# Kernel optimization log

Hardware: AMD Instinct MI355X
Metric: run time of the kernel (lower is better)

## Reference

```python
import jax, jax.numpy as jnp
import numpy as np

HS = 2048   # hidden_size
NH = 16     # num_attention_heads
HD = HS // NH  # head_dim = 128
FD = 256    # feature_dim
EPS = 1e-5  # layer_norm_epsilon


def setup_inputs() -> dict:
    key = jax.random.key(0)
    ks = jax.random.split(key, 12)
    s = 0.02
    return {
        "hidden_states": jax.random.normal(ks[0], (2, 4096, HS), jnp.float32),
        "attention_mask": jnp.zeros((2, 4096), jnp.float32),
        "Wq": jax.random.normal(ks[1], (HS, HS), jnp.float32) * s,
        "bq": jnp.zeros((HS,), jnp.float32),
        "Wk": jax.random.normal(ks[2], (HS, HS), jnp.float32) * s,
        "bk": jnp.zeros((HS,), jnp.float32),
        "Wv": jax.random.normal(ks[3], (HS, HS), jnp.float32) * s,
        "bv": jnp.zeros((HS,), jnp.float32),
        "Wo": jax.random.normal(ks[4], (HS, HS), jnp.float32) * s,
        "bo": jnp.zeros((HS,), jnp.float32),
        "Wf1": jax.random.normal(ks[5], (HD, FD), jnp.float32) * s,
        "bf1": jnp.zeros((FD,), jnp.float32),
        "Wf2": jax.random.normal(ks[6], (FD, FD), jnp.float32) * s,
        "bf2": jnp.zeros((FD,), jnp.float32),
        "ln_g": jnp.ones((FD,), jnp.float32),
        "ln_b": jnp.zeros((FD,), jnp.float32),
    }


def reference(hidden_states, attention_mask, Wq, bq, Wk, bk, Wv, bv, Wo, bo,
              Wf1, bf1, Wf2, bf2, ln_g, ln_b):
    B, L, H = hidden_states.shape

    # QKV projections -> [B, NH, L, HD]
    q = (hidden_states @ Wq + bq).reshape(B, L, NH, HD).transpose(0, 2, 1, 3)
    k = (hidden_states @ Wk + bk).reshape(B, L, NH, HD).transpose(0, 2, 1, 3)
    v = (hidden_states @ Wv + bv).reshape(B, L, NH, HD).transpose(0, 2, 1, 3)

    # seq_len (4096) > linear_threshold (1024) -> linear attention branch
    def feature_map(x):  # Linear -> ReLU -> Linear -> LayerNorm
        h = jax.nn.relu(x @ Wf1 + bf1)
        h = h @ Wf2 + bf2
        mu = jnp.mean(h, axis=-1, keepdims=True)
        var = jnp.var(h, axis=-1, keepdims=True)  # biased, like torch LayerNorm
        return (h - mu) * jax.lax.rsqrt(var + EPS) * ln_g + ln_b

    q_feat = feature_map(q)  # [B, NH, L, FD]
    k_feat = feature_map(k)
    # attention_mask [B, L] -> k_feat * (1 + mask)
    k_feat = k_feat * (1.0 + attention_mask[:, None, :, None])

    kv = jnp.einsum('bhlf,bhld->bhfd', k_feat, v)          # [B, NH, FD, HD]
    attn = jnp.einsum('bhlf,bhfd->bhld', q_feat, kv)       # [B, NH, L, HD]
    k_sum = jnp.sum(k_feat, axis=2)                         # [B, NH, FD]
    denom = jnp.einsum('bhlf,bhf->bhl', q_feat, k_sum)[..., None]
    attn = attn / (denom + 1e-8)

    attn = attn.transpose(0, 2, 1, 3).reshape(B, L, H)
    return attn @ Wo + bo
```

## Files before the change

### kernel.cpp

```cpp
#include <hip/hip_runtime.h>

typedef unsigned short u16;
typedef unsigned int u32;
typedef __attribute__((ext_vector_type(8))) short bf16x8;
typedef __attribute__((ext_vector_type(4))) float f32x4;

#define B_ 2
#define L_ 4096
#define HS_ 2048
#define NH_ 16
#define HD_ 128
#define FD_ 256

__device__ __forceinline__ float bf2f(u16 u) { return __uint_as_float(((u32)u) << 16); }
__device__ __forceinline__ u16 f2bf(float f) {
    u32 x = __float_as_uint(f);
    return (u16)((x + 0x7fffu + ((x >> 16) & 1u)) >> 16);
}

__device__ __forceinline__ void llds16(const u16* g, u16* l) {
    __builtin_amdgcn_global_load_lds((const __attribute__((address_space(1))) void*)g,
                                     (__attribute__((address_space(3))) void*)l, 16, 0, 0);
}

__device__ __forceinline__ void gemm_mainloop(const u16* __restrict__ Ab, int lda,
                                              const u16* __restrict__ Bb, int ldb,
                                              int K, u16* As, u16* Bs, f32x4 (&acc)[4][4]) {
    const int tid  = threadIdx.x;
    const int lane = tid & 63;
    const int wave = tid >> 6;
    const int wm = wave >> 1, wn = wave & 1;

    f32x4 zero = {0.f, 0.f, 0.f, 0.f};
#pragma unroll
    for (int i = 0; i < 4; i++)
#pragma unroll
        for (int j = 0; j < 4; j++) acc[i][j] = zero;

    const int srow = lane >> 2;
    const int scol = (lane & 3) * 8;
    const u16* pa = Ab + (size_t)(wave * 32 + srow) * lda + scol;
    const u16* pb = Bb + (size_t)(wave * 32 + srow) * ldb + scol;
    u16* la = As + wave * 1024;
    u16* lb = Bs + wave * 1024;

    const int arow = (wm * 64 + (lane & 15)) * 32 + (lane >> 4) * 8;
    const int brow = (wn * 64 + (lane & 15)) * 32 + (lane >> 4) * 8;

    for (int k0 = 0; k0 < K; k0 += 32) {
        llds16(pa, la);
        llds16(pa + 16 * lda, la + 512);
        llds16(pb, lb);
        llds16(pb + 16 * ldb, lb + 512);
        pa += 32; pb += 32;
        __syncthreads();
        bf16x8 af[4], bg[4];
#pragma unroll
        for (int mt = 0; mt < 4; mt++) af[mt] = *(const bf16x8*)(As + arow + mt * 512);
#pragma unroll
        for (int nt = 0; nt < 4; nt++) bg[nt] = *(const bf16x8*)(Bs + brow + nt * 512);
#pragma unroll
        for (int mt = 0; mt < 4; mt++)
#pragma unroll
            for (int nt = 0; nt < 4; nt++)
                acc[mt][nt] = __builtin_amdgcn_mfma_f32_16x16x32_bf16(af[mt], bg[nt], acc[mt][nt], 0, 0, 0);
        __syncthreads();
    }
}

__global__ __launch_bounds__(256) void k_cvt(const float* __restrict__ src, u16* __restrict__ dst) {
    size_t i = ((size_t)blockIdx.x * 256 + threadIdx.x) * 8;
    float4 a = *(const float4*)(src + i);
    float4 b = *(const float4*)(src + i + 4);
    union { u16 h[8]; uint4 v; } o;
    o.h[0] = f2bf(a.x); o.h[1] = f2bf(a.y); o.h[2] = f2bf(a.z); o.h[3] = f2bf(a.w);
    o.h[4] = f2bf(b.x); o.h[5] = f2bf(b.y); o.h[6] = f2bf(b.z); o.h[7] = f2bf(b.w);
    *(uint4*)(dst + i) = o.v;
}

__global__ __launch_bounds__(256) void k_transpose(const float* Wq, const float* Wk, const float* Wv,
                                                   const float* Wo, const float* Wf1, const float* Wf2,
                                                   u16* Wqkv_t, u16* Wo_t, u16* Wf1_t, u16* Wf2_t) {
    const float* src; u16* dst; int R, C;
    switch (blockIdx.z) {
        case 0: src = Wq;  dst = Wqkv_t;                R = 2048; C = 2048; break;
        case 1: src = Wk;  dst = Wqkv_t + 2048 * 2048;  R = 2048; C = 2048; break;
        case 2: src = Wv;  dst = Wqkv_t + 2 * 2048 * 2048; R = 2048; C = 2048; break;
        case 3: src = Wo;  dst = Wo_t;                  R = 2048; C = 2048; break;
        case 4: src = Wf1; dst = Wf1_t;                 R = 128;  C = 256;  break;
        default: src = Wf2; dst = Wf2_t;                R = 256;  C = 256;  break;
    }
    int c0 = blockIdx.x * 32, r0 = blockIdx.y * 32;
    if (c0 >= C || r0 >= R) return;
    __shared__ u16 tile[32][33];
    int tx = threadIdx.x, ty = threadIdx.y;
    for (int i = ty; i < 32; i += 8) tile[i][tx] = f2bf(src[(size_t)(r0 + i) * C + c0 + tx]);
    __syncthreads();
    for (int i = ty; i < 32; i += 8) dst[(size_t)(c0 + i) * R + r0 + tx] = tile[tx][i];
}

#define QKV_BAR() { __builtin_amdgcn_sched_barrier(0); __builtin_amdgcn_s_barrier(); \
                    __builtin_amdgcn_sched_barrier(0); }
#define QKV_LGKM0() { asm volatile("s_waitcnt lgkmcnt(0)" ::: "memory"); \
                      __builtin_amdgcn_sched_barrier(0); }

__device__ __forceinline__ void mainloop256(const u16* __restrict__ Abase,
                                            const u16* __restrict__ Bbase,
                                            u16* LDS, f32x4 (&acc)[8][4]) {
    const int tid = threadIdx.x, lane = tid & 63, wave = tid >> 6;
    const int wm = wave >> 2, wn = wave & 3;

    int r0g, c0g, r1g, c1g;
    { int p = tid * 16; int s = p >> 10, q = p & 1023; q ^= ((q >> 9) & 1) << 5;
      r0g = (s >> 1) * 16 + (q >> 6); c0g = (s & 1) * 32 + ((q & 63) >> 1); }
    { int p = 8192 + tid * 16; int s = p >> 10, q = p & 1023; q ^= ((q >> 9) & 1) << 5;
      r1g = (s >> 1) * 16 + (q >> 6); c1g = (s & 1) * 32 + ((q & 63) >> 1); }
    const int voff0 = r0g * HS_ + c0g;
    const int voff1 = r1g * HS_ + c1g;

    int qby = (lane & 15) * 64 + (lane >> 4) * 16;
    qby ^= ((qby >> 9) & 1) << 5;
    const int qh = qby >> 1;

#define STG(G, soff, dstu) { \
    llds16((G) + (soff) + voff0, LDS + (dstu) + wave * 512); \
    llds16((G) + (soff) + voff1, LDS + (dstu) + 4096 + wave * 512); }

    const size_t a0 = 0, a1 = (size_t)128 * HS_;
    const size_t b0 = 0, b1 = (size_t)128 * HS_;

    STG(Bbase, b0, 32768); STG(Bbase, b1, 40960);
    STG(Abase, a0, 0);     STG(Abase, a1, 8192);
    STG(Bbase, b0 + 64, 49152); STG(Bbase, b1 + 64, 57344);
    STG(Abase, a0 + 64, 16384);
    asm volatile("s_waitcnt vmcnt(6)" ::: "memory");
    QKV_BAR();

    f32x4 zero = {0.f, 0.f, 0.f, 0.f};
#pragma unroll
    for (int i = 0; i < 8; i++)
#pragma unroll
        for (int j = 0; j < 4; j++) acc[i][j] = zero;

    const int NT = HS_ / 64;
    bf16x8 afr[4][2], bfr[4][2];
    for (int t = 0; t < NT; t++) {
        const int bsel = t & 1;
        const u16* Ah = LDS + bsel * 16384 + wm * 8192;
        const u16* Bh = LDS + 32768 + bsel * 16384 + (wn >> 1) * 8192;
        const int bg0 = (wn & 1) * 4;
        const size_t kc1 = (size_t)(t + 1) * 64, kc2 = (size_t)(t + 2) * 64;

#pragma unroll
        for (int mf = 0; mf < 4; mf++)
#pragma unroll
            for (int ks = 0; ks < 2; ks++)
                afr[mf][ks] = *(const bf16x8*)(Ah + (mf * 2 + ks) * 512 + qh);
#pragma unroll
        for (int nf = 0; nf < 4; nf++)
#pragma unroll
            for (int ks = 0; ks < 2; ks++)
                bfr[nf][ks] = *(const bf16x8*)(Bh + ((bg0 + nf) * 2 + ks) * 512 + qh);
        if (t + 1 < NT) STG(Abase, a1 + kc1, (bsel ^ 1) * 16384 + 8192);
        QKV_BAR();
        QKV_LGKM0();
        __builtin_amdgcn_s_setprio(1);
#pragma unroll
        for (int mf = 0; mf < 4; mf++)
#pragma unroll
            for (int nf = 0; nf < 2; nf++)
#pragma unroll
                for (int ks = 0; ks < 2; ks++)
                    acc[mf][nf] = __builtin_amdgcn_mfma_f32_16x16x32_bf16(afr[mf][ks], bfr[nf][ks], acc[mf][nf], 0, 0, 0);
        __builtin_amdgcn_s_setprio(0);
        QKV_BAR();
        if (t + 2 < NT) STG(Bbase, b0 + kc2, 32768 + bsel * 16384);
        QKV_BAR();
        __builtin_amdgcn_s_setprio(1);
#pragma unroll
        for (int mf = 0; mf < 4; mf++)
#pragma unroll
            for (int nf = 2; nf < 4; nf++)
#pragma unroll
                for (int ks = 0; ks < 2; ks++)
                    acc[mf][nf] = __builtin_amdgcn_mfma_f32_16x16x32_bf16(afr[mf][ks], bfr[nf][ks], acc[mf][nf], 0, 0, 0);
        __builtin_amdgcn_s_setprio(0);
        QKV_BAR();
#pragma unroll
        for (int mf = 0; mf < 4; mf++)
#pragma unroll
            for (int ks = 0; ks < 2; ks++)
                afr[mf][ks] = *(const bf16x8*)(Ah + ((mf + 4) * 2 + ks) * 512 + qh);
        if (t + 2 < NT) STG(Bbase, b1 + kc2, 32768 + bsel * 16384 + 8192);
        QKV_BAR();
        QKV_LGKM0();
        __builtin_amdgcn_s_setprio(1);
#pragma unroll
        for (int mf = 0; mf < 4; mf++)
#pragma unroll
            for (int nf = 0; nf < 2; nf++)
#pragma unroll
                for (int ks = 0; ks < 2; ks++)
                    acc[mf + 4][nf] = __builtin_amdgcn_mfma_f32_16x16x32_bf16(afr[mf][ks], bfr[nf][ks], acc[mf + 4][nf], 0, 0, 0);
        __builtin_amdgcn_s_setprio(0);
        QKV_BAR();
        if (t + 2 < NT) STG(Abase, a0 + kc2, bsel * 16384);
        QKV_BAR();
        __builtin_amdgcn_s_setprio(1);
#pragma unroll
        for (int mf = 0; mf < 4; mf++)
#pragma unroll
            for (int nf = 2; nf < 4; nf++)
#pragma unroll
                for (int ks = 0; ks < 2; ks++)
                    acc[mf + 4][nf] = __builtin_amdgcn_mfma_f32_16x16x32_bf16(afr[mf][ks], bfr[nf][ks], acc[mf + 4][nf], 0, 0, 0);
        __builtin_amdgcn_s_setprio(0);
        if (t + 2 < NT) { asm volatile("s_waitcnt vmcnt(6)" ::: "memory"); }
        else if (t + 1 < NT) { asm volatile("s_waitcnt vmcnt(0)" ::: "memory"); }
        QKV_BAR();
    }
#undef STG
}

__global__ __launch_bounds__(512, 2) void k_gemm_qkv(
        const u16* __restrict__ X, const u16* __restrict__ Wt,
        const float* __restrict__ bq, const float* __restrict__ bk, const float* __restrict__ bv,
        u16* __restrict__ qout, u16* __restrict__ kout, u16* __restrict__ vT) {
    __shared__ u16 LDS[65536];
    const int tid = threadIdx.x, lane = tid & 63, wave = tid >> 6;
    const int wm = wave >> 2, wn = wave & 3;

    const int xcd = blockIdx.x & 7, idx = blockIdx.x >> 3;
    const int nblk = idx >> 2;
    const int mblk = xcd * 4 + (idx & 3);
    const int mb = mblk * 256, nb = nblk * 256;

    f32x4 acc[8][4];
    mainloop256(X + (size_t)mb * HS_, Wt + (size_t)nb * HS_, LDS, acc);

    const int which = nblk >> 3;
    const int colbase = (nblk & 7) * 256;
    const int bi = mb >> 12, lb = mb & 4095;
    const float* bias = (which == 0) ? bq : (which == 1 ? bk : bv);
    const int rb = (lane >> 4) << 2, cl = lane & 15;

    if (which < 2) {
        u16* dst = (which == 0) ? qout : kout;
        const int bh0 = bi * NH_ + (colbase >> 7);
        for (int half = 0; half < 2; half++) {
            if (wm == half) {
#pragma unroll
                for (int nf = 0; nf < 4; nf++) {
                    float bvv = bias[colbase + wn * 64 + nf * 16 + cl];
#pragma unroll
                    for (int mf = 0; mf < 8; mf++)
#pragma unroll
                        for (int r = 0; r < 4; r++)
                            LDS[(mf * 16 + rb + r) * 264 + wn * 64 + nf * 16 + cl] =
                                f2bf(acc[mf][nf][r] + bvv);
                }
            }
            __syncthreads();
#pragma unroll
            for (int it = 0; it < 8; it++) {
                int row = (tid >> 5) + it * 16;
                int c8 = (tid & 31) * 8;
                uint2 lo = *(const uint2*)(LDS + row * 264 + c8);
                uint2 hi = *(const uint2*)(LDS + row * 264 + c8 + 4);
                uint4 val = make_uint4(lo.x, lo.y, hi.x, hi.y);
                u16* pp = dst + ((size_t)(bh0 + (c8 >> 7)) * L_ + lb + half * 128 + row) * HD_ + (c8 & 127);
                *(uint4*)pp = val;
            }
            __syncthreads();
        }
    } else {
        for (int half = 0; half < 2; half++) {
            if (wm == half) {
#pragma unroll
                for (int nf = 0; nf < 4; nf++) {
                    float bvv = bias[colbase + wn * 64 + nf * 16 + cl];
#pragma unroll
                    for (int mf = 0; mf < 8; mf++)
#pragma unroll
                        for (int r = 0; r < 4; r++)
                            LDS[(wn * 64 + nf * 16 + cl) * 136 + mf * 16 + rb + r] =
                                f2bf(acc[mf][nf][r] + bvv);
                }
            }
            __syncthreads();
#pragma unroll
            for (int it = 0; it < 8; it++) {
                int n = (tid >> 4) + it * 32;
                int c8 = (tid & 15) * 8;
                uint2 lo = *(const uint2*)(LDS + n * 136 + c8);
                uint2 hi = *(const uint2*)(LDS + n * 136 + c8 + 4);
                uint4 val = make_uint4(lo.x, lo.y, hi.x, hi.y);
                int cg = colbase + n;
                u16* pp = vT + ((size_t)(bi * NH_ + (cg >> 7)) * HD_ + (cg & 127)) * L_ + lb + half * 128 + c8;
                *(uint4*)pp = val;
            }
            __syncthreads();
        }
    }
}

__global__ __launch_bounds__(512, 2) void k_gemm_out(const u16* __restrict__ A, const u16* __restrict__ Wt,
                                                     const float* __restrict__ bo, float* __restrict__ out) {
    __shared__ u16 LDS[65536];
    const int lane = threadIdx.x & 63, wave = threadIdx.x >> 6;
    const int wm = wave >> 2, wn = wave & 3;

    const int xcd = blockIdx.x & 7, idx = blockIdx.x >> 3;
    const int nblk = idx >> 2;
    const int mblk = xcd * 4 + (idx & 3);
    const int mb = mblk * 256, nb = nblk * 256;

    f32x4 acc[8][4];
    mainloop256(A + (size_t)mb * HS_, Wt + (size_t)nb * HS_, LDS, acc);

    const int rb = (lane >> 4) << 2, cl = lane & 15;
#pragma unroll
    for (int nf = 0; nf < 4; nf++) {
        int n = nb + wn * 64 + nf * 16 + cl;
        float bvv = bo[n];
#pragma unroll
        for (int mf = 0; mf < 8; mf++) {
            int m = mb + wm * 128 + mf * 16 + rb;
#pragma unroll
            for (int r = 0; r < 4; r++)
                out[(size_t)(m + r) * HS_ + n] = acc[mf][nf][r] + bvv;
        }
    }
}

template <int MASKED, int TRANS>
__global__ __launch_bounds__(256) void k_feat(const u16* __restrict__ X,
                                              const u16* __restrict__ W1t, const float* __restrict__ b1,
                                              const u16* __restrict__ W2t, const float* __restrict__ b2,
                                              const float* __restrict__ g, const float* __restrict__ be,
                                              const float* __restrict__ mask,
                                              u16* __restrict__ feat, float* __restrict__ ksp) {
    __shared__ u16 As[64 * 32];
    __shared__ u16 Bs[256 * 32];
    __shared__ u16 H[64 * 264];
    __shared__ float MU[64], RS[64], FAC[64];
    const int tid = threadIdx.x, lane = tid & 63, wave = tid >> 6;
    const int mb = blockIdx.x * 64;

    const int srow = lane >> 2, scol = (lane & 3) * 8;
    const int arow_rd = (lane & 15);
    const int kgrp = (lane >> 4) * 8;

    f32x4 acc[4][4];
    f32x4 zero = {0.f, 0.f, 0.f, 0.f};
#pragma unroll
    for (int i = 0; i < 4; i++)
#pragma unroll
        for (int j = 0; j < 4; j++) acc[i][j] = zero;

    for (int k0 = 0; k0 < 128; k0 += 32) {
        llds16(X + (size_t)(mb + wave * 16 + srow) * 128 + k0 + scol, As + wave * 512);
#pragma unroll
        for (int i = 0; i < 4; i++)
            llds16(W1t + (size_t)((wave * 4 + i) * 16 + srow) * 128 + k0 + scol,
                   Bs + (wave * 4 + i) * 512);
        __syncthreads();
        bf16x8 af[4], bg[4];
#pragma unroll
        for (int mt = 0; mt < 4; mt++) af[mt] = *(const bf16x8*)(As + (mt * 16 + arow_rd) * 32 + kgrp);
#pragma unroll
        for (int nt = 0; nt < 4; nt++) bg[nt] = *(const bf16x8*)(Bs + (wave * 64 + nt * 16 + arow_rd) * 32 + kgrp);
#pragma unroll
        for (int mt = 0; mt < 4; mt++)
#pragma unroll
            for (int nt = 0; nt < 4; nt++)
                acc[mt][nt] = __builtin_amdgcn_mfma_f32_16x16x32_bf16(af[mt], bg[nt], acc[mt][nt], 0, 0, 0);
        __syncthreads();
    }
    {
        const int rbase = (lane >> 4) << 2;
#pragma unroll
        for (int nt = 0; nt < 4; nt++) {
            int n = wave * 64 + nt * 16 + (lane & 15);
            float bvv = b1[n];
#pragma unroll
            for (int mt = 0; mt < 4; mt++)
#pragma unroll
                for (int r = 0; r < 4; r++) {
                    float v = fmaxf(acc[mt][nt][r] + bvv, 0.f);
                    H[(mt * 16 + rbase + r) * 264 + n] = f2bf(v);
                }
            acc[0][nt] = zero; acc[1][nt] = zero; acc[2][nt] = zero; acc[3][nt] = zero;
        }
    }
    __syncthreads();

    for (int k0 = 0; k0 < 256; k0 += 32) {
#pragma unroll
        for (int i = 0; i < 4; i++)
            llds16(W2t + (size_t)((wave * 4 + i) * 16 + srow) * 256 + k0 + scol,
                   Bs + (wave * 4 + i) * 512);
        __syncthreads();
        bf16x8 af[4], bg[4];
#pragma unroll
        for (int mt = 0; mt < 4; mt++) af[mt] = *(const bf16x8*)(H + (mt * 16 + arow_rd) * 264 + k0 + kgrp);
#pragma unroll
        for (int nt = 0; nt < 4; nt++) bg[nt] = *(const bf16x8*)(Bs + (wave * 64 + nt * 16 + arow_rd) * 32 + kgrp);
#pragma unroll
        for (int mt = 0; mt < 4; mt++)
#pragma unroll
            for (int nt = 0; nt < 4; nt++)
                acc[mt][nt] = __builtin_amdgcn_mfma_f32_16x16x32_bf16(af[mt], bg[nt], acc[mt][nt], 0, 0, 0);
        __syncthreads();
    }
    {
        const int rbase = (lane >> 4) << 2;
#pragma unroll
        for (int nt = 0; nt < 4; nt++) {
            int n = wave * 64 + nt * 16 + (lane & 15);
            float bvv = b2[n];
#pragma unroll
            for (int mt = 0; mt < 4; mt++)
#pragma unroll
                for (int r = 0; r < 4; r++)
                    H[(mt * 16 + rbase + r) * 264 + n] = f2bf(acc[mt][nt][r] + bvv);
        }
    }
    __syncthreads();

    {
        for (int r = 0; r < 16; r++) {
            int row = wave * 16 + r;
            int j = lane * 4;
            uint2 u = *(const uint2*)(H + row * 264 + j);
            float x0 = bf2f((u16)(u.x & 0xffff)), x1 = bf2f((u16)(u.x >> 16));
            float x2 = bf2f((u16)(u.y & 0xffff)), x3 = bf2f((u16)(u.y >> 16));
            float s = x0 + x1 + x2 + x3;
            float ss = x0 * x0 + x1 * x1 + x2 * x2 + x3 * x3;
#pragma unroll
            for (int o = 32; o >= 1; o >>= 1) { s += __shfl_xor(s, o); ss += __shfl_xor(ss, o); }
            if (lane == 0) {
                float mu = s * (1.f / FD_);
                float var = ss * (1.f / FD_) - mu * mu;
                MU[row] = mu;
                RS[row] = rsqrtf(var + 1e-5f);
                float fac = 1.f;
                if (MASKED) {
                    int grow = mb + row;
                    int b = grow >> 16;
                    int l = grow & 4095;
                    fac = 1.f + mask[b * L_ + l];
                }
                FAC[row] = fac;
            }
        }
    }
    __syncthreads();

    if (!TRANS) {
        int j = lane * 4;
        float4 gg = *(const float4*)(g + j);
        float4 bb = *(const float4*)(be + j);
        for (int r = 0; r < 16; r++) {
            int row = wave * 16 + r;
            float mu = MU[row], rstd = RS[row], fac = FAC[row];
            uint2 u = *(const uint2*)(H + row * 264 + j);
            float x0 = bf2f((u16)(u.x & 0xffff)), x1 = bf2f((u16)(u.x >> 16));
            float x2 = bf2f((u16)(u.y & 0xffff)), x3 = bf2f((u16)(u.y >> 16));
            uint2 o2;
            o2.x = (u32)f2bf(((x0 - mu) * rstd * gg.x + bb.x) * fac) |
                   ((u32)f2bf(((x1 - mu) * rstd * gg.y + bb.y) * fac) << 16);
            o2.y = (u32)f2bf(((x2 - mu) * rstd * gg.z + bb.z) * fac) |
                   ((u32)f2bf(((x3 - mu) * rstd * gg.w + bb.w) * fac) << 16);
            *(uint2*)(feat + (size_t)(mb + row) * FD_ + j) = o2;
        }
    } else {
        int f = tid;
        int bh = mb >> 12, lb = mb & 4095;
        float gf = g[f], bf = be[f];
        u16* orow = feat + ((size_t)bh * FD_ + f) * L_ + lb;
        float fsum = 0.f;
        for (int lg = 0; lg < 64; lg += 8) {
            union { u16 h8[8]; uint4 v4; } pk;
#pragma unroll
            for (int j = 0; j < 8; j++) {
                int row = lg + j;
                float x = bf2f(H[row * 264 + f]);
                float y = ((x - MU[row]) * RS[row] * gf + bf) * FAC[row];
                fsum += y;
                pk.h8[j] = f2bf(y);
            }
            *(uint4*)(orow + lg) = pk.v4;
        }
        ksp[((size_t)bh * 64 + (lb >> 6)) * FD_ + f] = fsum;
    }
}

__global__ __launch_bounds__(256) void k_ksum2(const float* __restrict__ ksp, float* __restrict__ ksum) {
    const int bh = blockIdx.x, f = threadIdx.x;
    float s = 0.f;
    for (int i = 0; i < 64; i++) s += ksp[((size_t)bh * 64 + i) * FD_ + f];
    ksum[(size_t)bh * FD_ + f] = s;
}

__global__ __launch_bounds__(256) void k_gemm_kv(const u16* __restrict__ kfT, const u16* __restrict__ vT,
                                                 float* __restrict__ kvp) {
    __shared__ u16 As[4096], Bs[4096];
    f32x4 acc[4][4];
    const int mb = blockIdx.x * 128;
    const int ks = blockIdx.y;
    const int bh = blockIdx.z;
    gemm_mainloop(kfT + ((size_t)bh * FD_ + mb) * L_ + ks * 512, L_,
                  vT + (size_t)bh * HD_ * L_ + ks * 512, L_, 512, As, Bs, acc);
    const int lane = threadIdx.x & 63, wave = threadIdx.x >> 6;
    const int wm = wave >> 1, wn = wave & 1;
    const int n0 = wn * 64 + (lane & 15);
    const int m0 = mb + wm * 64 + ((lane >> 4) << 2);
    float* o = kvp + (size_t)(ks * 32 + bh) * (FD_ * HD_);
#pragma unroll
    for (int nt = 0; nt < 4; nt++)
#pragma unroll
        for (int mt = 0; mt < 4; mt++)
#pragma unroll
            for (int r = 0; r < 4; r++)
                o[(size_t)(m0 + mt * 16 + r) * HD_ + n0 + nt * 16] = acc[mt][nt][r];
}

__global__ __launch_bounds__(256) void k_kvred(const float* __restrict__ kvp, u16* __restrict__ kvT) {
    const int p = blockIdx.x, bh = blockIdx.y, t = threadIdx.x;
    const int e0 = p * 4096 + t * 16;
    float s[16];
#pragma unroll
    for (int i = 0; i < 16; i++) s[i] = 0.f;
    for (int c = 0; c < 8; c++) {
        const float* src = kvp + ((size_t)(c * 32 + bh)) * 32768 + e0;
#pragma unroll
        for (int i = 0; i < 16; i += 4) {
            float4 vv = *(const float4*)(src + i);
            s[i] += vv.x; s[i + 1] += vv.y; s[i + 2] += vv.z; s[i + 3] += vv.w;
        }
    }
#pragma unroll
    for (int i = 0; i < 16; i++) {
        int e = e0 + i, fq = e >> 7, d = e & 127;
        kvT[((size_t)bh * HD_ + d) * FD_ + fq] = f2bf(s[i]);
    }
}

__global__ __launch_bounds__(256) void k_denom(const u16* __restrict__ qf, const float* __restrict__ ksum,
                                               float* __restrict__ denom) {
    const int lane = threadIdx.x & 63, wave = threadIdx.x >> 6;
    const size_t row0 = (size_t)blockIdx.x * 16 + wave * 4;
    const int bh = (int)(row0 >> 12);
    float4 kk = *(const float4*)(ksum + (size_t)bh * FD_ + lane * 4);
#pragma unroll
    for (int rr = 0; rr < 4; rr++) {
        size_t row = row0 + rr;
        uint2 u = *(const uint2*)(qf + row * FD_ + lane * 4);
        float d = bf2f((u16)(u.x & 0xffff)) * kk.x + bf2f((u16)(u.x >> 16)) * kk.y
                + bf2f((u16)(u.y & 0xffff)) * kk.z + bf2f((u16)(u.y >> 16)) * kk.w;
#pragma unroll
        for (int o = 32; o >= 1; o >>= 1) d += __shfl_xor(d, o);
        if (lane == 0) denom[row] = d;
    }
}

__global__ __launch_bounds__(256) void k_gemm_attn(const u16* __restrict__ qf, const u16* __restrict__ kvT,
                                                   const float* __restrict__ denom, u16* __restrict__ attn) {
    __shared__ u16 S[128 * 132];
    f32x4 acc[4][4];
    const int mb = blockIdx.x * 128;
    const int bh = blockIdx.y;
    gemm_mainloop(qf + ((size_t)bh * L_ + mb) * FD_, FD_, kvT + (size_t)bh * HD_ * FD_, FD_, FD_, S, S + 4096, acc);
    const int tid = threadIdx.x, lane = tid & 63, wave = tid >> 6;
    const int wm = wave >> 1, wn = wave & 1;
    const int b = bh >> 4, h = bh & 15;
    const int mloc = wm * 64 + ((lane >> 4) << 2);
    const int nloc = wn * 64 + (lane & 15);
#pragma unroll
    for (int mt = 0; mt < 4; mt++)
#pragma unroll
        for (int r = 0; r < 4; r++) {
            int l = mb + mloc + mt * 16 + r;
            float rden = 1.f / (denom[(size_t)bh * L_ + l] + 1e-8f);
#pragma unroll
            for (int nt = 0; nt < 4; nt++)
                S[(mloc + mt * 16 + r) * 132 + nloc + nt * 16] = f2bf(acc[mt][nt][r] * rden);
        }
    __syncthreads();
    const int c8 = (tid & 15) * 8;
#pragma unroll
    for (int it = 0; it < 8; it++) {
        int row = (tid >> 4) + it * 16;
        uint2 lo = *(const uint2*)(S + row * 132 + c8);
        uint2 hi = *(const uint2*)(S + row * 132 + c8 + 4);
        uint4 val = make_uint4(lo.x, lo.y, hi.x, hi.y);
        *(uint4*)(attn + ((size_t)(b * L_ + mb + row)) * HS_ + h * HD_ + c8) = val;
    }
}

extern "C" void kernel_launch(void* const* d_in, const int* in_sizes, int n_in,
                              void* d_out, int out_size, void* d_ws, size_t ws_size,
                              hipStream_t stream) {
    const float* hs  = (const float*)d_in[0];
    const float* msk = (const float*)d_in[1];
    const float* Wq  = (const float*)d_in[2];  const float* bq  = (const float*)d_in[3];
    const float* Wk  = (const float*)d_in[4];  const float* bk  = (const float*)d_in[5];
    const float* Wv  = (const float*)d_in[6];  const float* bv  = (const float*)d_in[7];
    const float* Wo  = (const float*)d_in[8];  const float* bo  = (const float*)d_in[9];
    const float* Wf1 = (const float*)d_in[10]; const float* bf1 = (const float*)d_in[11];
    const float* Wf2 = (const float*)d_in[12]; const float* bf2 = (const float*)d_in[13];
    const float* lng = (const float*)d_in[14]; const float* lnb = (const float*)d_in[15];
    float* out = (float*)d_out;
    char* w = (char*)d_ws;

    u16* qfeat  = (u16*)(w + 0);
    u16* Wqkv_t = (u16*)(w + 0);
    u16* Xbf    = (u16*)(w + 25165824u);
    u16* kfT    = (u16*)(w + 67108864u);
    u16* qbuf   = (u16*)(w + 134217728u);
    float* kvp  = (float*)(w + 134217728u);
    u16* kbuf   = (u16*)(w + 167772160u);
    u16* attn   = (u16*)(w + 167772160u);
    u16* vT     = (u16*)(w + 201326592u);
    u16* Wo_t   = (u16*)(w + 234881024u);
    u16* Wf1_t  = (u16*)(w + 243269632u);
    u16* Wf2_t  = (u16*)(w + 243335168u);
    float* ksp  = (float*)(w + 243466240u);
    u16* kvT    = (u16*)(w + 245563392u);
    float* ksum = (float*)(w + 247660544u);
    float* denom = (float*)(w + 247693312u);

    k_cvt<<<dim3(8192), 256, 0, stream>>>(hs, Xbf);
    k_transpose<<<dim3(64, 64, 6), dim3(32, 8), 0, stream>>>(Wq, Wk, Wv, Wo, Wf1, Wf2,
                                                             Wqkv_t, Wo_t, Wf1_t, Wf2_t);
    k_gemm_qkv<<<dim3(768), 512, 0, stream>>>(Xbf, Wqkv_t, bq, bk, bv, qbuf, kbuf, vT);
    k_feat<0, 0><<<dim3(2048), 256, 0, stream>>>(qbuf, Wf1_t, bf1, Wf2_t, bf2, lng, lnb, msk, qfeat, ksp);
    k_feat<1, 1><<<dim3(2048), 256, 0, stream>>>(kbuf, Wf1_t, bf1, Wf2_t, bf2, lng, lnb, msk, kfT, ksp);
    k_ksum2<<<dim3(32), 256, 0, stream>>>(ksp, ksum);
    k_gemm_kv<<<dim3(2, 8, 32), 256, 0, stream>>>(kfT, vT, kvp);
    k_kvred<<<dim3(8, 32), 256, 0, stream>>>(kvp, kvT);
    k_denom<<<dim3(8192), 256, 0, stream>>>(qfeat, ksum, denom);
    k_gemm_attn<<<dim3(32, 32), 256, 0, stream>>>(qfeat, kvT, denom, attn);
    k_gemm_out<<<dim3(256), 512, 0, stream>>>(attn, Wo_t, bo, out);
}
```

Measured before the change: 699.0 us.

## Fuse denominator into query feature kernel and rewrite attention GEMM with full-K LDS

The query feature-map kernel now runs after the key-sum is ready, so it can compute the per-row denominator dot product in its LayerNorm epilogue. This removes the separate k_denom pass and its re-read of qfeat. The attention GEMM is rewritten to use 512 threads and load the whole K=256 tiles of qfeat and kvT into LDS in a single burst with swizzled addressing, instead of the shared mainloop. The kvp buffer is moved so it no longer overlaps qbuf, which the reordered query feature launch still reads. In exchange, the attention GEMM uses 128KB of LDS, which limits occupancy, and the feature kernel does extra cross-lane reductions.

```diff
diff --git a/kernel.cpp b/kernel.cpp
--- a/kernel.cpp
+++ b/kernel.cpp
@@ -338,8 +338,9 @@
                                               const u16* __restrict__ W1t, const float* __restrict__ b1,
                                               const u16* __restrict__ W2t, const float* __restrict__ b2,
                                               const float* __restrict__ g, const float* __restrict__ be,
-                                              const float* __restrict__ mask,
-                                              u16* __restrict__ feat, float* __restrict__ ksp) {
+                                              const float* __restrict__ mask, const float* __restrict__ ksum,
+                                              u16* __restrict__ feat, float* __restrict__ ksp,
+                                              float* __restrict__ denomOut) {
     __shared__ u16 As[64 * 32];
     __shared__ u16 Bs[256 * 32];
     __shared__ u16 H[64 * 264];
@@ -461,18 +462,25 @@
         int j = lane * 4;
         float4 gg = *(const float4*)(g + j);
         float4 bb = *(const float4*)(be + j);
+        float4 kk = *(const float4*)(ksum + (size_t)(mb >> 12) * FD_ + j);
         for (int r = 0; r < 16; r++) {
             int row = wave * 16 + r;
             float mu = MU[row], rstd = RS[row], fac = FAC[row];
             uint2 u = *(const uint2*)(H + row * 264 + j);
             float x0 = bf2f((u16)(u.x & 0xffff)), x1 = bf2f((u16)(u.x >> 16));
             float x2 = bf2f((u16)(u.y & 0xffff)), x3 = bf2f((u16)(u.y >> 16));
+            u16 h0 = f2bf(((x0 - mu) * rstd * gg.x + bb.x) * fac);
+            u16 h1 = f2bf(((x1 - mu) * rstd * gg.y + bb.y) * fac);
+            u16 h2 = f2bf(((x2 - mu) * rstd * gg.z + bb.z) * fac);
+            u16 h3 = f2bf(((x3 - mu) * rstd * gg.w + bb.w) * fac);
             uint2 o2;
-            o2.x = (u32)f2bf(((x0 - mu) * rstd * gg.x + bb.x) * fac) |
-                   ((u32)f2bf(((x1 - mu) * rstd * gg.y + bb.y) * fac) << 16);
-            o2.y = (u32)f2bf(((x2 - mu) * rstd * gg.z + bb.z) * fac) |
-                   ((u32)f2bf(((x3 - mu) * rstd * gg.w + bb.w) * fac) << 16);
+            o2.x = (u32)h0 | ((u32)h1 << 16);
+            o2.y = (u32)h2 | ((u32)h3 << 16);
             *(uint2*)(feat + (size_t)(mb + row) * FD_ + j) = o2;
+            float dp = bf2f(h0) * kk.x + bf2f(h1) * kk.y + bf2f(h2) * kk.z + bf2f(h3) * kk.w;
+#pragma unroll
+            for (int o = 32; o >= 1; o >>= 1) dp += __shfl_xor(dp, o);
+            if (lane == 0) denomOut[mb + row] = dp;
         }
     } else {
         int f = tid;
@@ -547,53 +555,85 @@
     }
 }
 
-__global__ __launch_bounds__(256) void k_denom(const u16* __restrict__ qf, const float* __restrict__ ksum,
-                                               float* __restrict__ denom) {
-    const int lane = threadIdx.x & 63, wave = threadIdx.x >> 6;
-    const size_t row0 = (size_t)blockIdx.x * 16 + wave * 4;
-    const int bh = (int)(row0 >> 12);
-    float4 kk = *(const float4*)(ksum + (size_t)bh * FD_ + lane * 4);
-#pragma unroll
-    for (int rr = 0; rr < 4; rr++) {
-        size_t row = row0 + rr;
-        uint2 u = *(const uint2*)(qf + row * FD_ + lane * 4);
-        float d = bf2f((u16)(u.x & 0xffff)) * kk.x + bf2f((u16)(u.x >> 16)) * kk.y
-                + bf2f((u16)(u.y & 0xffff)) * kk.z + bf2f((u16)(u.y >> 16)) * kk.w;
-#pragma unroll
-        for (int o = 32; o >= 1; o >>= 1) d += __shfl_xor(d, o);
-        if (lane == 0) denom[row] = d;
-    }
-}
-
-__global__ __launch_bounds__(256) void k_gemm_attn(const u16* __restrict__ qf, const u16* __restrict__ kvT,
-                                                   const float* __restrict__ denom, u16* __restrict__ attn) {
-    __shared__ u16 S[128 * 132];
-    f32x4 acc[4][4];
+__global__ __launch_bounds__(512, 2) void k_gemm_attn(const u16* __restrict__ qf, const u16* __restrict__ kvT,
+                                                      const float* __restrict__ denom, u16* __restrict__ attn) {
+    __shared__ u16 LDS[65536];
+    const int tid = threadIdx.x, lane = tid & 63, wave = tid >> 6;
+    const int wm = wave >> 2, wn = wave & 3;
     const int mb = blockIdx.x * 128;
     const int bh = blockIdx.y;
-    gemm_mainloop(qf + ((size_t)bh * L_ + mb) * FD_, FD_, kvT + (size_t)bh * HD_ * FD_, FD_, FD_, S, S + 4096, acc);
-    const int tid = threadIdx.x, lane = tid & 63, wave = tid >> 6;
-    const int wm = wave >> 1, wn = wave & 1;
+
+    int r0g, c0g, r1g, c1g;
+    { int p = tid * 16; int s = p >> 10, q = p & 1023; q ^= ((q >> 9) & 1) << 5;
+      r0g = (s >> 1) * 16 + (q >> 6); c0g = (s & 1) * 32 + ((q & 63) >> 1); }
+    { int p = 8192 + tid * 16; int s = p >> 10, q = p & 1023; q ^= ((q >> 9) & 1) << 5;
+      r1g = (s >> 1) * 16 + (q >> 6); c1g = (s & 1) * 32 + ((q & 63) >> 1); }
+    const int voff0 = r0g * FD_ + c0g;
+    const int voff1 = r1g * FD_ + c1g;
+
+    int qby = (lane & 15) * 64 + (lane >> 4) * 16;
+    qby ^= ((qby >> 9) & 1) << 5;
+    const int qh = qby >> 1;
+
+    const u16* Ab = qf + ((size_t)bh * L_ + mb) * FD_;
+    const u16* Bb = kvT + (size_t)bh * HD_ * FD_;
+#pragma unroll
+    for (int hg = 0; hg < 4; hg++) {
+        llds16(Ab + hg * 64 + voff0, LDS + hg * 8192 + wave * 512);
+        llds16(Ab + hg * 64 + voff1, LDS + hg * 8192 + 4096 + wave * 512);
+        llds16(Bb + hg * 64 + voff0, LDS + 32768 + hg * 8192 + wave * 512);
+        llds16(Bb + hg * 64 + voff1, LDS + 32768 + hg * 8192 + 4096 + wave * 512);
+    }
+    asm volatile("s_waitcnt vmcnt(0)" ::: "memory");
+    __syncthreads();
+
+    f32x4 acc[4][2];
+    f32x4 zero = {0.f, 0.f, 0.f, 0.f};
+#pragma unroll
+    for (int i = 0; i < 4; i++) { acc[i][0] = zero; acc[i][1] = zero; }
+
+#pragma unroll
+    for (int kg = 0; kg < 4; kg++) {
+        bf16x8 af[4][2], bg[2][2];
+#pragma unroll
+        for (int mt = 0; mt < 4; mt++)
+#pragma unroll
+            for (int ks = 0; ks < 2; ks++)
+                af[mt][ks] = *(const bf16x8*)(LDS + kg * 8192 + ((wm * 4 + mt) * 2 + ks) * 512 + qh);
+#pragma unroll
+        for (int nt = 0; nt < 2; nt++)
+#pragma unroll
+            for (int ks = 0; ks < 2; ks++)
+                bg[nt][ks] = *(const bf16x8*)(LDS + 32768 + kg * 8192 + ((wn * 2 + nt) * 2 + ks) * 512 + qh);
+#pragma unroll
+        for (int mt = 0; mt < 4; mt++)
+#pragma unroll
+            for (int nt = 0; nt < 2; nt++)
+#pragma unroll
+                for (int ks = 0; ks < 2; ks++)
+                    acc[mt][nt] = __builtin_amdgcn_mfma_f32_16x16x32_bf16(af[mt][ks], bg[nt][ks], acc[mt][nt], 0, 0, 0);
+    }
+    __syncthreads();
+
+    const int rb = (lane >> 4) << 2, cl = lane & 15;
+#pragma unroll
+    for (int mt = 0; mt < 4; mt++)
+#pragma unroll
+        for (int r = 0; r < 4; r++) {
+            int row = wm * 64 + mt * 16 + rb + r;
+            float rden = 1.f / (denom[(size_t)bh * L_ + mb + row] + 1e-8f);
+#pragma unroll
+            for (int nt = 0; nt < 2; nt++)
+                LDS[row * 132 + wn * 32 + nt * 16 + cl] = f2bf(acc[mt][nt][r] * rden);
+        }
+    __syncthreads();
     const int b = bh >> 4, h = bh & 15;
-    const int mloc = wm * 64 + ((lane >> 4) << 2);
-    const int nloc = wn * 64 + (lane & 15);
-#pragma unroll
-    for (int mt = 0; mt < 4; mt++)
-#pragma unroll
-        for (int r = 0; r < 4; r++) {
-            int l = mb + mloc + mt * 16 + r;
-            float rden = 1.f / (denom[(size_t)bh * L_ + l] + 1e-8f);
-#pragma unroll
-            for (int nt = 0; nt < 4; nt++)
-                S[(mloc + mt * 16 + r) * 132 + nloc + nt * 16] = f2bf(acc[mt][nt][r] * rden);
-        }
-    __syncthreads();
     const int c8 = (tid & 15) * 8;
 #pragma unroll
-    for (int it = 0; it < 8; it++) {
-        int row = (tid >> 4) + it * 16;
-        uint2 lo = *(const uint2*)(S + row * 132 + c8);
-        uint2 hi = *(const uint2*)(S + row * 132 + c8 + 4);
+    for (int it = 0; it < 4; it++) {
+        int row = (tid >> 4) + it * 32;
+        uint2 lo = *(const uint2*)(LDS + row * 132 + c8);
+        uint2 hi = *(const uint2*)(LDS + row * 132 + c8 + 4);
         uint4 val = make_uint4(lo.x, lo.y, hi.x, hi.y);
         *(uint4*)(attn + ((size_t)(b * L_ + mb + row)) * HS_ + h * HD_ + c8) = val;
     }
@@ -619,8 +659,8 @@
     u16* Xbf    = (u16*)(w + 25165824u);
     u16* kfT    = (u16*)(w + 67108864u);
     u16* qbuf   = (u16*)(w + 134217728u);
-    float* kvp  = (float*)(w + 134217728u);
     u16* kbuf   = (u16*)(w + 167772160u);
+    float* kvp  = (float*)(w + 167772160u);
     u16* attn   = (u16*)(w + 167772160u);
     u16* vT     = (u16*)(w + 201326592u);
     u16* Wo_t   = (u16*)(w + 234881024u);
@@ -635,12 +675,13 @@
     k_transpose<<<dim3(64, 64, 6), dim3(32, 8), 0, stream>>>(Wq, Wk, Wv, Wo, Wf1, Wf2,
                                                              Wqkv_t, Wo_t, Wf1_t, Wf2_t);
     k_gemm_qkv<<<dim3(768), 512, 0, stream>>>(Xbf, Wqkv_t, bq, bk, bv, qbuf, kbuf, vT);
-    k_feat<0, 0><<<dim3(2048), 256, 0, stream>>>(qbuf, Wf1_t, bf1, Wf2_t, bf2, lng, lnb, msk, qfeat, ksp);
-    k_feat<1, 1><<<dim3(2048), 256, 0, stream>>>(kbuf, Wf1_t, bf1, Wf2_t, bf2, lng, lnb, msk, kfT, ksp);
+    k_feat<1, 1><<<dim3(2048), 256, 0, stream>>>(kbuf, Wf1_t, bf1, Wf2_t, bf2, lng, lnb, msk,
+                                                 nullptr, kfT, ksp, nullptr);
     k_ksum2<<<dim3(32), 256, 0, stream>>>(ksp, ksum);
     k_gemm_kv<<<dim3(2, 8, 32), 256, 0, stream>>>(kfT, vT, kvp);
     k_kvred<<<dim3(8, 32), 256, 0, stream>>>(kvp, kvT);
-    k_denom<<<dim3(8192), 256, 0, stream>>>(qfeat, ksum, denom);
-    k_gemm_attn<<<dim3(32, 32), 256, 0, stream>>>(qfeat, kvT, denom, attn);
+    k_feat<0, 0><<<dim3(2048), 256, 0, stream>>>(qbuf, Wf1_t, bf1, Wf2_t, bf2, lng, lnb, msk,
+                                                 ksum, qfeat, ksp, denom);
+    k_gemm_attn<<<dim3(32, 32), 512, 0, stream>>>(qfeat, kvT, denom, attn);
     k_gemm_out<<<dim3(256), 512, 0, stream>>>(attn, Wo_t, bo, out);
 }
```

New measurement: 695.7 us. About the same (-0.5%).

## Fuse query feature map, denominator and attention GEMM into one kernel

Applied to the files above, without the earlier changes.

The query feature-map kernel now keeps its LayerNorm output in shared memory, computes the per-row denominator against ksum, and multiplies by kvT with MFMA to write the normalized attention output directly. This removes the qfeat and denom round trips through global memory and drops two kernel launches. The key path is reordered to run first so ksum and kvT exist beforehand. The KV split-K is also halved from 8 to 4 chunks, giving fewer partials to reduce but less parallelism.

```diff
diff --git a/kernel.cpp b/kernel.cpp
--- a/kernel.cpp
+++ b/kernel.cpp
@@ -338,12 +338,14 @@
                                               const u16* __restrict__ W1t, const float* __restrict__ b1,
                                               const u16* __restrict__ W2t, const float* __restrict__ b2,
                                               const float* __restrict__ g, const float* __restrict__ be,
-                                              const float* __restrict__ mask,
-                                              u16* __restrict__ feat, float* __restrict__ ksp) {
+                                              const float* __restrict__ mask, const float* __restrict__ ksum,
+                                              const u16* __restrict__ kvT,
+                                              u16* __restrict__ feat, float* __restrict__ ksp,
+                                              u16* __restrict__ attnOut) {
     __shared__ u16 As[64 * 32];
     __shared__ u16 Bs[256 * 32];
     __shared__ u16 H[64 * 264];
-    __shared__ float MU[64], RS[64], FAC[64];
+    __shared__ float MU[64], RS[64], FAC[64], RD[64];
     const int tid = threadIdx.x, lane = tid & 63, wave = tid >> 6;
     const int mb = blockIdx.x * 64;
 
@@ -458,21 +460,66 @@
     __syncthreads();
 
     if (!TRANS) {
-        int j = lane * 4;
-        float4 gg = *(const float4*)(g + j);
-        float4 bb = *(const float4*)(be + j);
-        for (int r = 0; r < 16; r++) {
-            int row = wave * 16 + r;
-            float mu = MU[row], rstd = RS[row], fac = FAC[row];
-            uint2 u = *(const uint2*)(H + row * 264 + j);
-            float x0 = bf2f((u16)(u.x & 0xffff)), x1 = bf2f((u16)(u.x >> 16));
-            float x2 = bf2f((u16)(u.y & 0xffff)), x3 = bf2f((u16)(u.y >> 16));
-            uint2 o2;
-            o2.x = (u32)f2bf(((x0 - mu) * rstd * gg.x + bb.x) * fac) |
-                   ((u32)f2bf(((x1 - mu) * rstd * gg.y + bb.y) * fac) << 16);
-            o2.y = (u32)f2bf(((x2 - mu) * rstd * gg.z + bb.z) * fac) |
-                   ((u32)f2bf(((x3 - mu) * rstd * gg.w + bb.w) * fac) << 16);
-            *(uint2*)(feat + (size_t)(mb + row) * FD_ + j) = o2;
+        const int bh = mb >> 12;
+        {
+            int j = lane * 4;
+            float4 gg = *(const float4*)(g + j);
+            float4 bb = *(const float4*)(be + j);
+            float4 kk = *(const float4*)(ksum + (size_t)bh * FD_ + j);
+            for (int r = 0; r < 16; r++) {
+                int row = wave * 16 + r;
+                float mu = MU[row], rstd = RS[row], fac = FAC[row];
+                uint2 u = *(const uint2*)(H + row * 264 + j);
+                float x0 = bf2f((u16)(u.x & 0xffff)), x1 = bf2f((u16)(u.x >> 16));
+                float x2 = bf2f((u16)(u.y & 0xffff)), x3 = bf2f((u16)(u.y >> 16));
+                u16 h0 = f2bf(((x0 - mu) * rstd * gg.x + bb.x) * fac);
+                u16 h1 = f2bf(((x1 - mu) * rstd * gg.y + bb.y) * fac);
+                u16 h2 = f2bf(((x2 - mu) * rstd * gg.z + bb.z) * fac);
+                u16 h3 = f2bf(((x3 - mu) * rstd * gg.w + bb.w) * fac);
+                uint2 o2;
+                o2.x = (u32)h0 | ((u32)h1 << 16);
+                o2.y = (u32)h2 | ((u32)h3 << 16);
+                *(uint2*)(H + row * 264 + j) = o2;
+                float dp = bf2f(h0) * kk.x + bf2f(h1) * kk.y + bf2f(h2) * kk.z + bf2f(h3) * kk.w;
+#pragma unroll
+                for (int o = 32; o >= 1; o >>= 1) dp += __shfl_xor(dp, o);
+                if (lane == 0) RD[row] = 1.f / (dp + 1e-8f);
+            }
+        }
+        const u16* kvTb = kvT + (size_t)bh * HD_ * FD_;
+        f32x4 pacc[8];
+#pragma unroll
+        for (int i = 0; i < 8; i++) pacc[i] = zero;
+        for (int k0 = 0; k0 < 256; k0 += 32) {
+            llds16(kvTb + (size_t)(wave * 32 + srow) * FD_ + k0 + scol, Bs + (wave * 32) * 32);
+            llds16(kvTb + (size_t)(wave * 32 + 16 + srow) * FD_ + k0 + scol, Bs + (wave * 32 + 16) * 32);
+            __syncthreads();
+            bf16x8 af = *(const bf16x8*)(H + (wave * 16 + arow_rd) * 264 + k0 + kgrp);
+#pragma unroll
+            for (int nt = 0; nt < 8; nt++) {
+                bf16x8 bg = *(const bf16x8*)(Bs + (nt * 16 + arow_rd) * 32 + kgrp);
+                pacc[nt] = __builtin_amdgcn_mfma_f32_16x16x32_bf16(af, bg, pacc[nt], 0, 0, 0);
+            }
+            __syncthreads();
+        }
+        const int rbase = (lane >> 4) << 2, cl = lane & 15;
+#pragma unroll
+        for (int nt = 0; nt < 8; nt++)
+#pragma unroll
+            for (int r = 0; r < 4; r++) {
+                int row = wave * 16 + rbase + r;
+                H[row * 264 + nt * 16 + cl] = f2bf(pacc[nt][r] * RD[row]);
+            }
+        __syncthreads();
+        const int b = bh >> 4, h = bh & 15, lb = mb & 4095;
+        const int c8 = (tid & 15) * 8;
+#pragma unroll
+        for (int it = 0; it < 4; it++) {
+            int row = (tid >> 4) + it * 16;
+            uint2 lo = *(const uint2*)(H + row * 264 + c8);
+            uint2 hi = *(const uint2*)(H + row * 264 + c8 + 4);
+            *(uint4*)(attnOut + ((size_t)(b * L_ + lb + row)) * HS_ + h * HD_ + c8) =
+                make_uint4(lo.x, lo.y, hi.x, hi.y);
         }
     } else {
         int f = tid;
@@ -510,8 +557,8 @@
     const int mb = blockIdx.x * 128;
     const int ks = blockIdx.y;
     const int bh = blockIdx.z;
-    gemm_mainloop(kfT + ((size_t)bh * FD_ + mb) * L_ + ks * 512, L_,
-                  vT + (size_t)bh * HD_ * L_ + ks * 512, L_, 512, As, Bs, acc);
+    gemm_mainloop(kfT + ((size_t)bh * FD_ + mb) * L_ + ks * 1024, L_,
+                  vT + (size_t)bh * HD_ * L_ + ks * 1024, L_, 1024, As, Bs, acc);
     const int lane = threadIdx.x & 63, wave = threadIdx.x >> 6;
     const int wm = wave >> 1, wn = wave & 1;
     const int n0 = wn * 64 + (lane & 15);
@@ -532,7 +579,7 @@
     float s[16];
 #pragma unroll
     for (int i = 0; i < 16; i++) s[i] = 0.f;
-    for (int c = 0; c < 8; c++) {
+    for (int c = 0; c < 4; c++) {
         const float* src = kvp + ((size_t)(c * 32 + bh)) * 32768 + e0;
 #pragma unroll
         for (int i = 0; i < 16; i += 4) {
@@ -544,58 +591,6 @@
     for (int i = 0; i < 16; i++) {
         int e = e0 + i, fq = e >> 7, d = e & 127;
         kvT[((size_t)bh * HD_ + d) * FD_ + fq] = f2bf(s[i]);
-    }
-}
-
-__global__ __launch_bounds__(256) void k_denom(const u16* __restrict__ qf, const float* __restrict__ ksum,
-                                               float* __restrict__ denom) {
-    const int lane = threadIdx.x & 63, wave = threadIdx.x >> 6;
-    const size_t row0 = (size_t)blockIdx.x * 16 + wave * 4;
-    const int bh = (int)(row0 >> 12);
-    float4 kk = *(const float4*)(ksum + (size_t)bh * FD_ + lane * 4);
-#pragma unroll
-    for (int rr = 0; rr < 4; rr++) {
-        size_t row = row0 + rr;
-        uint2 u = *(const uint2*)(qf + row * FD_ + lane * 4);
-        float d = bf2f((u16)(u.x & 0xffff)) * kk.x + bf2f((u16)(u.x >> 16)) * kk.y
-                + bf2f((u16)(u.y & 0xffff)) * kk.z + bf2f((u16)(u.y >> 16)) * kk.w;
-#pragma unroll
-        for (int o = 32; o >= 1; o >>= 1) d += __shfl_xor(d, o);
-        if (lane == 0) denom[row] = d;
-    }
-}
-
-__global__ __launch_bounds__(256) void k_gemm_attn(const u16* __restrict__ qf, const u16* __restrict__ kvT,
-                                                   const float* __restrict__ denom, u16* __restrict__ attn) {
-    __shared__ u16 S[128 * 132];
-    f32x4 acc[4][4];
-    const int mb = blockIdx.x * 128;
-    const int bh = blockIdx.y;
-    gemm_mainloop(qf + ((size_t)bh * L_ + mb) * FD_, FD_, kvT + (size_t)bh * HD_ * FD_, FD_, FD_, S, S + 4096, acc);
-    const int tid = threadIdx.x, lane = tid & 63, wave = tid >> 6;
-    const int wm = wave >> 1, wn = wave & 1;
-    const int b = bh >> 4, h = bh & 15;
-    const int mloc = wm * 64 + ((lane >> 4) << 2);
-    const int nloc = wn * 64 + (lane & 15);
-#pragma unroll
-    for (int mt = 0; mt < 4; mt++)
-#pragma unroll
-        for (int r = 0; r < 4; r++) {
-            int l = mb + mloc + mt * 16 + r;
-            float rden = 1.f / (denom[(size_t)bh * L_ + l] + 1e-8f);
-#pragma unroll
-            for (int nt = 0; nt < 4; nt++)
-                S[(mloc + mt * 16 + r) * 132 + nloc + nt * 16] = f2bf(acc[mt][nt][r] * rden);
-        }
-    __syncthreads();
-    const int c8 = (tid & 15) * 8;
-#pragma unroll
-    for (int it = 0; it < 8; it++) {
-        int row = (tid >> 4) + it * 16;
-        uint2 lo = *(const uint2*)(S + row * 132 + c8);
-        uint2 hi = *(const uint2*)(S + row * 132 + c8 + 4);
-        uint4 val = make_uint4(lo.x, lo.y, hi.x, hi.y);
-        *(uint4*)(attn + ((size_t)(b * L_ + mb + row)) * HS_ + h * HD_ + c8) = val;
     }
 }
 
@@ -614,13 +609,12 @@
     float* out = (float*)d_out;
     char* w = (char*)d_ws;
 
-    u16* qfeat  = (u16*)(w + 0);
     u16* Wqkv_t = (u16*)(w + 0);
     u16* Xbf    = (u16*)(w + 25165824u);
     u16* kfT    = (u16*)(w + 67108864u);
     u16* qbuf   = (u16*)(w + 134217728u);
-    float* kvp  = (float*)(w + 134217728u);
     u16* kbuf   = (u16*)(w + 167772160u);
+    float* kvp  = (float*)(w + 167772160u);
     u16* attn   = (u16*)(w + 167772160u);
     u16* vT     = (u16*)(w + 201326592u);
     u16* Wo_t   = (u16*)(w + 234881024u);
@@ -629,18 +623,17 @@
     float* ksp  = (float*)(w + 243466240u);
     u16* kvT    = (u16*)(w + 245563392u);
     float* ksum = (float*)(w + 247660544u);
-    float* denom = (float*)(w + 247693312u);
 
     k_cvt<<<dim3(8192), 256, 0, stream>>>(hs, Xbf);
     k_transpose<<<dim3(64, 64, 6), dim3(32, 8), 0, stream>>>(Wq, Wk, Wv, Wo, Wf1, Wf2,
                                                              Wqkv_t, Wo_t, Wf1_t, Wf2_t);
     k_gemm_qkv<<<dim3(768), 512, 0, stream>>>(Xbf, Wqkv_t, bq, bk, bv, qbuf, kbuf, vT);
-    k_feat<0, 0><<<dim3(2048), 256, 0, stream>>>(qbuf, Wf1_t, bf1, Wf2_t, bf2, lng, lnb, msk, qfeat, ksp);
-    k_feat<1, 1><<<dim3(2048), 256, 0, stream>>>(kbuf, Wf1_t, bf1, Wf2_t, bf2, lng, lnb, msk, kfT, ksp);
+    k_feat<1, 1><<<dim3(2048), 256, 0, stream>>>(kbuf, Wf1_t, bf1, Wf2_t, bf2, lng, lnb, msk,
+                                                 nullptr, nullptr, kfT, ksp, nullptr);
     k_ksum2<<<dim3(32), 256, 0, stream>>>(ksp, ksum);
-    k_gemm_kv<<<dim3(2, 8, 32), 256, 0, stream>>>(kfT, vT, kvp);
+    k_gemm_kv<<<dim3(2, 4, 32), 256, 0, stream>>>(kfT, vT, kvp);
     k_kvred<<<dim3(8, 32), 256, 0, stream>>>(kvp, kvT);
-    k_denom<<<dim3(8192), 256, 0, stream>>>(qfeat, ksum, denom);
-    k_gemm_attn<<<dim3(32, 32), 256, 0, stream>>>(qfeat, kvT, denom, attn);
+    k_feat<0, 0><<<dim3(2048), 256, 0, stream>>>(qbuf, Wf1_t, bf1, Wf2_t, bf2, lng, lnb, msk,
+                                                 ksum, kvT, nullptr, nullptr, attn);
     k_gemm_out<<<dim3(256), 512, 0, stream>>>(attn, Wo_t, bo, out);
 }
```

New measurement: 673.1 us. 1.04x faster.
